# Optimization experiments

Hardware: AMD Instinct MI355X
Metric: run time of the kernel (lower is better)

Reference implementation:

```python
import jax, jax.numpy as jnp
import numpy as np

# ---- init_kwargs-derived constants ----
B, IN_F, OUT_F = 8192, 4096, 4096
W_SCALE = 0.01          # layer_params['w_scale']
B_SCALE = 0.01          # layer_params['b_scale']
IN_MIN, IN_MAX = -1.0, 1.0   # input_stats
NUM_BITS = 8
QMAX = 2 ** NUM_BITS - 1
IN_SCALE = (IN_MAX - IN_MIN) / QMAX
IN_ZP = int(round(-IN_MIN / (IN_SCALE + 1e-12)))


def setup_inputs() -> dict:
    key = jax.random.key(0)
    k1, k2, k3 = jax.random.split(key, 3)
    x_float = jax.random.normal(k1, (B, IN_F), dtype=jnp.float32)
    # int8-range weights/bias (stored as int32 containers)
    w_q = jax.random.randint(k2, (OUT_F, IN_F), -128, 128, dtype=jnp.int32)
    b_q = jax.random.randint(k3, (OUT_F,), -128, 128, dtype=jnp.int32)
    return {"x_float": x_float, "w_q": w_q, "b_q": b_q}


def reference(x_float, w_q, b_q):
    # quantize input to uint8 range [0,255]
    x_q = jnp.clip(jnp.round(x_float / IN_SCALE + IN_ZP), 0, 255).astype(jnp.int32)
    x_shifted = x_q - IN_ZP                       # [B, IN_F] int32
    # exact int32 accumulation matmul: [B, IN_F] @ [IN_F, OUT_F]
    acc_int = jnp.matmul(x_shifted, w_q.T, preferred_element_type=jnp.int32)
    out = acc_int.astype(jnp.float32) * (IN_SCALE * W_SCALE)
    out = out + b_q.astype(jnp.float32) * B_SCALE  # bias_float = b_q * b_scale
    return out
```

## Files before the change

### kernel.cpp

```cpp
#include <hip/hip_runtime.h>
#include <stdint.h>

constexpr int Mdim = 8192;
constexpr int Ndim = 4096;
constexpr int Kdim = 4096;

#define ISF        ((float)(2.0 / 255.0))
#define OUT_SCALE  ((float)(2.0 / 255.0 * 0.01))
#define BSCALE     0.01f

typedef int i32x4 __attribute__((ext_vector_type(4)));

__global__ __launch_bounds__(256) void quantize_x(const float* __restrict__ x,
                                                  int* __restrict__ x8,
                                                  int ngroups) {
  int idx = blockIdx.x * 256 + threadIdx.x;
  int stride = gridDim.x * 256;
  for (int g = idx; g < ngroups; g += stride) {
    float4 v = reinterpret_cast<const float4*>(x)[g];
    int a0 = (int)rintf(v.x / ISF + 127.0f);
    int a1 = (int)rintf(v.y / ISF + 127.0f);
    int a2 = (int)rintf(v.z / ISF + 127.0f);
    int a3 = (int)rintf(v.w / ISF + 127.0f);
    a0 = a0 < 0 ? 0 : (a0 > 255 ? 255 : a0); a0 -= 128;
    a1 = a1 < 0 ? 0 : (a1 > 255 ? 255 : a1); a1 -= 128;
    a2 = a2 < 0 ? 0 : (a2 > 255 ? 255 : a2); a2 -= 128;
    a3 = a3 < 0 ? 0 : (a3 > 255 ? 255 : a3); a3 -= 128;
    x8[g] = (a0 & 0xff) | ((a1 & 0xff) << 8) | ((a2 & 0xff) << 16) |
            (int)(((unsigned)(a3 & 0xff)) << 24);
  }
}

__global__ __launch_bounds__(256) void convert_w(const int* __restrict__ wq,
                                                 int* __restrict__ w8,
                                                 int* __restrict__ wsum) {
  int row = blockIdx.x;
  const int4* src = reinterpret_cast<const int4*>(wq + (size_t)row * Kdim);
  int* dst = w8 + (size_t)row * (Kdim / 4);
  int s = 0;
#pragma unroll
  for (int i = 0; i < 4; ++i) {
    int idx = i * 256 + threadIdx.x;
    int4 v = src[idx];
    s += v.x + v.y + v.z + v.w;
    dst[idx] = (v.x & 0xff) | ((v.y & 0xff) << 8) | ((v.z & 0xff) << 16) |
               (int)(((unsigned)(v.w & 0xff)) << 24);
  }
  __shared__ int red[256];
  red[threadIdx.x] = s;
  __syncthreads();
  for (int off = 128; off; off >>= 1) {
    if ((int)threadIdx.x < off) red[threadIdx.x] += red[threadIdx.x + off];
    __syncthreads();
  }
  if (threadIdx.x == 0) wsum[row] = red[0];
}

__global__ __launch_bounds__(256) void gemm_i8(const int8_t* __restrict__ A8,
                                               const int8_t* __restrict__ B8,
                                               const int* __restrict__ wsum,
                                               const int* __restrict__ bq,
                                               float* __restrict__ out) {
  __shared__ uint8_t lds[32768];

  int bid = blockIdx.x;
  int wg = (bid & 7) * 256 + (bid >> 3);
  int bm = wg >> 5;
  int bn = wg & 31;

  const int tid = threadIdx.x;
  const int lane = tid & 63;
  const int wv = tid >> 6;
  const int l15 = lane & 15, hi = lane >> 4;
  const int wr = wv >> 1, wc = wv & 1;
  const int sw = l15 & 7;

  size_t aSrc[4], bSrc[4];
  int ldsOff[4];
#pragma unroll
  for (int it = 0; it < 4; ++it) {
    int e = it * 256 + tid;
    int r = e >> 3, s = e & 7;
    int col = (s ^ (r & 7)) << 4;
    aSrc[it] = (size_t)(bm * 128 + r) * Kdim + col;
    bSrc[it] = (size_t)(bn * 128 + r) * Kdim + col;
    ldsOff[it] = it * 4096 + wv * 1024;
  }

  int aRow[4], bRow[4];
#pragma unroll
  for (int i = 0; i < 4; ++i) {
    aRow[i] = (wr * 64 + i * 16 + l15) * 128;
    bRow[i] = 16384 + (wc * 64 + i * 16 + l15) * 128;
  }

  i32x4 acc[4][4] = {};

  for (int kt = 0; kt < Kdim / 128; ++kt) {
#pragma unroll
    for (int it = 0; it < 4; ++it)
      __builtin_amdgcn_global_load_lds(
          (const __attribute__((address_space(1))) void*)(A8 + aSrc[it] + (size_t)kt * 128),
          (__attribute__((address_space(3))) void*)(&lds[ldsOff[it]]), 16, 0, 0);
#pragma unroll
    for (int it = 0; it < 4; ++it)
      __builtin_amdgcn_global_load_lds(
          (const __attribute__((address_space(1))) void*)(B8 + bSrc[it] + (size_t)kt * 128),
          (__attribute__((address_space(3))) void*)(&lds[16384 + ldsOff[it]]), 16, 0, 0);
    __syncthreads();

#pragma unroll
    for (int ks = 0; ks < 2; ++ks) {
      i32x4 a[4], b[4];
#pragma unroll
      for (int i = 0; i < 4; ++i)
        a[i] = *reinterpret_cast<const i32x4*>(&lds[aRow[i] + ((((ks << 2) + hi) ^ sw) << 4)]);
#pragma unroll
      for (int j = 0; j < 4; ++j)
        b[j] = *reinterpret_cast<const i32x4*>(&lds[bRow[j] + ((((ks << 2) + hi) ^ sw) << 4)]);
#pragma unroll
      for (int i = 0; i < 4; ++i)
#pragma unroll
        for (int j = 0; j < 4; ++j)
          acc[i][j] = __builtin_amdgcn_mfma_i32_16x16x64_i8(a[i], b[j], acc[i][j], 0, 0, 0);
    }
    __syncthreads();
  }

  float fb[4];
  int ws4[4];
#pragma unroll
  for (int j = 0; j < 4; ++j) {
    int c = bn * 128 + wc * 64 + j * 16 + l15;
    fb[j] = (float)bq[c] * BSCALE;
    ws4[j] = wsum[c];
  }
#pragma unroll
  for (int i = 0; i < 4; ++i) {
    int rbase = bm * 128 + wr * 64 + i * 16 + hi * 4;
#pragma unroll
    for (int p = 0; p < 4; ++p) {
      size_t ro = (size_t)(rbase + p) * Ndim + bn * 128 + wc * 64;
#pragma unroll
      for (int j = 0; j < 4; ++j)
        out[ro + j * 16 + l15] = (float)(acc[i][j][p] + ws4[j]) * OUT_SCALE + fb[j];
    }
  }
}

__global__ void fallback_kernel(const float* __restrict__ x, const int* __restrict__ wq,
                                const int* __restrict__ bq, float* __restrict__ out) {
  int col = blockIdx.x * 16 + (threadIdx.x & 15);
  int row = blockIdx.y * 16 + (threadIdx.x >> 4);
  const float* xr = x + (size_t)row * Kdim;
  const int* wr_ = wq + (size_t)col * Kdim;
  int acc = 0;
  for (int k = 0; k < Kdim; ++k) {
    int v = (int)rintf(xr[k] / ISF + 127.0f);
    v = v < 0 ? 0 : (v > 255 ? 255 : v);
    acc += (v - 127) * wr_[k];
  }
  out[(size_t)row * Ndim + col] = (float)acc * OUT_SCALE + (float)bq[col] * BSCALE;
}

extern "C" void kernel_launch(void* const* d_in, const int* in_sizes, int n_in,
                              void* d_out, int out_size, void* d_ws, size_t ws_size,
                              hipStream_t stream) {
  const float* x = (const float*)d_in[0];
  const int* wq = (const int*)d_in[1];
  const int* bq = (const int*)d_in[2];
  float* out = (float*)d_out;

  const size_t x8_bytes = (size_t)Mdim * Kdim;
  const size_t w8_bytes = (size_t)Ndim * Kdim;
  const size_t ws_need = x8_bytes + w8_bytes + (size_t)Ndim * sizeof(int);

  if (ws_size >= ws_need) {
    int8_t* x8 = (int8_t*)d_ws;
    int8_t* w8 = x8 + x8_bytes;
    int* wsum = (int*)(w8 + w8_bytes);

    quantize_x<<<2048, 256, 0, stream>>>(x, (int*)x8, Mdim * Kdim / 4);
    convert_w<<<Ndim, 256, 0, stream>>>(wq, (int*)w8, wsum);
    gemm_i8<<<(Mdim / 128) * (Ndim / 128), 256, 0, stream>>>(x8, w8, wsum, bq, out);
  } else {
    dim3 grid(Ndim / 16, Mdim / 16);
    fallback_kernel<<<grid, 256, 0, stream>>>(x, wq, bq, out);
  }
}
```

Measured before the change: 221.2 us.

## Rewrite int8 GEMM as 256x256 tile, double-buffered 8-phase pipelined kernel

Replaces the 128x128, 256-thread int8 GEMM with a 256x256 tile, 512-thread kernel. It uses 128KB of double-buffered LDS and splits each K tile into four phases. Prefetches for the next B tile and the A tile two steps ahead are issued between MFMA phases, paced with explicit vmcnt waits, barriers and s_setprio. The aim is to raise data reuse per loaded byte and hide global-to-LDS latency behind matrix work. The cost is much higher register and LDS pressure: one block per CU and only 512 workgroups, so about two waves across the device.

```diff
diff --git a/kernel.cpp b/kernel.cpp
--- a/kernel.cpp
+++ b/kernel.cpp
@@ -4,6 +4,7 @@
 constexpr int Mdim = 8192;
 constexpr int Ndim = 4096;
 constexpr int Kdim = 4096;
+constexpr int NT = Kdim / 128;
 
 #define ISF        ((float)(2.0 / 255.0))
 #define OUT_SCALE  ((float)(2.0 / 255.0 * 0.01))
@@ -56,96 +57,135 @@
   if (threadIdx.x == 0) wsum[row] = red[0];
 }
 
-__global__ __launch_bounds__(256) void gemm_i8(const int8_t* __restrict__ A8,
-                                               const int8_t* __restrict__ B8,
-                                               const int* __restrict__ wsum,
-                                               const int* __restrict__ bq,
-                                               float* __restrict__ out) {
-  __shared__ uint8_t lds[32768];
+#define AS1C const __attribute__((address_space(1))) void*
+#define AS3  __attribute__((address_space(3))) void*
+#define GLL(src, dst) __builtin_amdgcn_global_load_lds((AS1C)(src), (AS3)(dst), 16, 0, 0)
+#define BAR() asm volatile("s_barrier" ::: "memory")
+#define MFMA(a, b, c) __builtin_amdgcn_mfma_i32_16x16x64_i8(a, b, c, 0, 0, 0)
+
+__global__ __launch_bounds__(512) void gemm_i8_8ph(const int8_t* __restrict__ A8,
+                                                   const int8_t* __restrict__ B8,
+                                                   const int* __restrict__ wsum,
+                                                   const int* __restrict__ bq,
+                                                   float* __restrict__ out) {
+  __shared__ uint8_t lds[131072];
 
   int bid = blockIdx.x;
-  int wg = (bid & 7) * 256 + (bid >> 3);
-  int bm = wg >> 5;
-  int bn = wg & 31;
+  int wg = (bid & 7) * 64 + (bid >> 3);
+  int bm = wg >> 4;
+  int bn = wg & 15;
 
   const int tid = threadIdx.x;
   const int lane = tid & 63;
   const int wv = tid >> 6;
+  const int wr = wv >> 2;
+  const int wc = wv & 3;
   const int l15 = lane & 15, hi = lane >> 4;
-  const int wr = wv >> 1, wc = wv & 1;
-  const int sw = l15 & 7;
-
-  size_t aSrc[4], bSrc[4];
-  int ldsOff[4];
-#pragma unroll
-  for (int it = 0; it < 4; ++it) {
-    int e = it * 256 + tid;
-    int r = e >> 3, s = e & 7;
-    int col = (s ^ (r & 7)) << 4;
-    aSrc[it] = (size_t)(bm * 128 + r) * Kdim + col;
-    bSrc[it] = (size_t)(bn * 128 + r) * Kdim + col;
-    ldsOff[it] = it * 4096 + wv * 1024;
-  }
-
-  int aRow[4], bRow[4];
-#pragma unroll
-  for (int i = 0; i < 4; ++i) {
-    aRow[i] = (wr * 64 + i * 16 + l15) * 128;
-    bRow[i] = 16384 + (wc * 64 + i * 16 + l15) * 128;
-  }
-
-  i32x4 acc[4][4] = {};
-
-  for (int kt = 0; kt < Kdim / 128; ++kt) {
-#pragma unroll
-    for (int it = 0; it < 4; ++it)
-      __builtin_amdgcn_global_load_lds(
-          (const __attribute__((address_space(1))) void*)(A8 + aSrc[it] + (size_t)kt * 128),
-          (__attribute__((address_space(3))) void*)(&lds[ldsOff[it]]), 16, 0, 0);
-#pragma unroll
-    for (int it = 0; it < 4; ++it)
-      __builtin_amdgcn_global_load_lds(
-          (const __attribute__((address_space(1))) void*)(B8 + bSrc[it] + (size_t)kt * 128),
-          (__attribute__((address_space(3))) void*)(&lds[16384 + ldsOff[it]]), 16, 0, 0);
-    __syncthreads();
-
-#pragma unroll
-    for (int ks = 0; ks < 2; ++ks) {
-      i32x4 a[4], b[4];
-#pragma unroll
-      for (int i = 0; i < 4; ++i)
-        a[i] = *reinterpret_cast<const i32x4*>(&lds[aRow[i] + ((((ks << 2) + hi) ^ sw) << 4)]);
-#pragma unroll
-      for (int j = 0; j < 4; ++j)
-        b[j] = *reinterpret_cast<const i32x4*>(&lds[bRow[j] + ((((ks << 2) + hi) ^ sw) << 4)]);
-#pragma unroll
-      for (int i = 0; i < 4; ++i)
-#pragma unroll
-        for (int j = 0; j < 4; ++j)
-          acc[i][j] = __builtin_amdgcn_mfma_i32_16x16x64_i8(a[i], b[j], acc[i][j], 0, 0, 0);
+
+  const int r3 = lane >> 3, s3 = lane & 7;
+  const int swcol = (s3 ^ r3) << 4;
+  const size_t aoff = (size_t)(bm * 256 + wv * 8 + r3) * Kdim + swcol;
+  const size_t boff = (size_t)(bn * 256 + wv * 8 + r3) * Kdim + swcol;
+  const int ldsw = wv * 1024;
+
+#define ISSUE_A(P, t, half) do { \
+    GLL(A8 + aoff + (size_t)(t) * 128 + (size_t)((half) * 128) * Kdim, \
+        &lds[(P) * 32768 + (half) * 16384 + ldsw]); \
+    GLL(A8 + aoff + (size_t)(t) * 128 + (size_t)((half) * 128 + 64) * Kdim, \
+        &lds[(P) * 32768 + (half) * 16384 + 8192 + ldsw]); \
+  } while (0)
+#define ISSUE_B(P, t, half) do { \
+    GLL(B8 + boff + (size_t)(t) * 128 + (size_t)((half) * 128) * Kdim, \
+        &lds[65536 + (P) * 32768 + (half) * 16384 + ldsw]); \
+    GLL(B8 + boff + (size_t)(t) * 128 + (size_t)((half) * 128 + 64) * Kdim, \
+        &lds[65536 + (P) * 32768 + (half) * 16384 + 8192 + ldsw]); \
+  } while (0)
+
+  const int aRow = (wr * 128 + l15) * 128;
+  const int bRow = (wc * 64 + l15) * 128;
+  const int sl0 = (hi ^ (l15 & 7)) << 4;
+  const int sl1 = ((4 + hi) ^ (l15 & 7)) << 4;
+
+#define LDA(P, i, ks) (*reinterpret_cast<const i32x4*>( \
+    &lds[(P) * 32768 + aRow + (i) * 2048 + ((ks) ? sl1 : sl0)]))
+#define LDB(P, j, ks) (*reinterpret_cast<const i32x4*>( \
+    &lds[65536 + (P) * 32768 + bRow + (j) * 2048 + ((ks) ? sl1 : sl0)]))
+
+  i32x4 acc[8][4];
+#pragma unroll
+  for (int i = 0; i < 8; ++i)
+#pragma unroll
+    for (int j = 0; j < 4; ++j) acc[i][j] = (i32x4){0, 0, 0, 0};
+
+  ISSUE_A(0, 0, 0); ISSUE_A(0, 0, 1);
+  ISSUE_B(0, 0, 0); ISSUE_B(0, 0, 1);
+  ISSUE_A(1, 1, 0); ISSUE_A(1, 1, 1);
+  asm volatile("s_waitcnt vmcnt(4)" ::: "memory");
+  BAR();
+
+#define KTILE(P, t, DOB, DOA, VM4, VM0) do { \
+    i32x4 a0[8], a1[8], bb0, bb1; \
+     \
+    if (DOB) ISSUE_B((P) ^ 1, (t) + 1, 0); \
+    bb0 = LDB(P, 0, 0); bb1 = LDB(P, 1, 0); \
+    _Pragma("unroll") for (int i = 0; i < 8; ++i) a0[i] = LDA(P, i, 0); \
+    BAR(); __builtin_amdgcn_s_setprio(1); \
+    _Pragma("unroll") for (int i = 0; i < 8; ++i) { \
+      acc[i][0] = MFMA(a0[i], bb0, acc[i][0]); acc[i][1] = MFMA(a0[i], bb1, acc[i][1]); } \
+    __builtin_amdgcn_s_setprio(0); BAR(); \
+     \
+    if (DOB) ISSUE_B((P) ^ 1, (t) + 1, 1); \
+    bb0 = LDB(P, 2, 0); bb1 = LDB(P, 3, 0); \
+    _Pragma("unroll") for (int i = 0; i < 8; ++i) a1[i] = LDA(P, i, 1); \
+    BAR(); __builtin_amdgcn_s_setprio(1); \
+    _Pragma("unroll") for (int i = 0; i < 8; ++i) { \
+      acc[i][2] = MFMA(a0[i], bb0, acc[i][2]); acc[i][3] = MFMA(a0[i], bb1, acc[i][3]); } \
+    __builtin_amdgcn_s_setprio(0); BAR(); \
+     \
+    if (DOA) ISSUE_A(P, (t) + 2, 0); \
+    bb0 = LDB(P, 0, 1); bb1 = LDB(P, 1, 1); \
+    BAR(); __builtin_amdgcn_s_setprio(1); \
+    _Pragma("unroll") for (int i = 0; i < 8; ++i) { \
+      acc[i][0] = MFMA(a1[i], bb0, acc[i][0]); acc[i][1] = MFMA(a1[i], bb1, acc[i][1]); } \
+    __builtin_amdgcn_s_setprio(0); BAR(); \
+     \
+    if (DOA) ISSUE_A(P, (t) + 2, 1); \
+    bb0 = LDB(P, 2, 1); bb1 = LDB(P, 3, 1); \
+    BAR(); __builtin_amdgcn_s_setprio(1); \
+    _Pragma("unroll") for (int i = 0; i < 8; ++i) { \
+      acc[i][2] = MFMA(a1[i], bb0, acc[i][2]); acc[i][3] = MFMA(a1[i], bb1, acc[i][3]); } \
+    __builtin_amdgcn_s_setprio(0); \
+    if (VM4) asm volatile("s_waitcnt vmcnt(4)" ::: "memory"); \
+    if (VM0) asm volatile("s_waitcnt vmcnt(0)" ::: "memory"); \
+    BAR(); \
+  } while (0)
+
+  for (int it = 0; it < NT / 2 - 1; ++it) {
+    int ta = 2 * it, tb = 2 * it + 1;
+    KTILE(0, ta, 1, 1, 1, 0);
+    KTILE(1, tb, 1, 1, 1, 0);
+  }
+  KTILE(0, 30, 1, 0, 0, 1);
+  KTILE(1, 31, 0, 0, 0, 0);
+
+#pragma unroll
+  for (int j = 0; j < 4; ++j) {
+    int col = bn * 256 + wc * 64 + j * 16 + l15;
+    float fb = (float)bq[col] * BSCALE;
+    int ws = wsum[col];
+#pragma unroll
+    for (int i = 0; i < 8; ++i) {
+      int rbase = bm * 256 + wr * 128 + i * 16 + hi * 4;
+#pragma unroll
+      for (int p = 0; p < 4; ++p)
+        out[(size_t)(rbase + p) * Ndim + col] = (float)(acc[i][j][p] + ws) * OUT_SCALE + fb;
     }
-    __syncthreads();
-  }
-
-  float fb[4];
-  int ws4[4];
-#pragma unroll
-  for (int j = 0; j < 4; ++j) {
-    int c = bn * 128 + wc * 64 + j * 16 + l15;
-    fb[j] = (float)bq[c] * BSCALE;
-    ws4[j] = wsum[c];
-  }
-#pragma unroll
-  for (int i = 0; i < 4; ++i) {
-    int rbase = bm * 128 + wr * 64 + i * 16 + hi * 4;
-#pragma unroll
-    for (int p = 0; p < 4; ++p) {
-      size_t ro = (size_t)(rbase + p) * Ndim + bn * 128 + wc * 64;
-#pragma unroll
-      for (int j = 0; j < 4; ++j)
-        out[ro + j * 16 + l15] = (float)(acc[i][j][p] + ws4[j]) * OUT_SCALE + fb[j];
-    }
-  }
+  }
+#undef KTILE
+#undef ISSUE_A
+#undef ISSUE_B
+#undef LDA
+#undef LDB
 }
 
 __global__ void fallback_kernel(const float* __restrict__ x, const int* __restrict__ wq,
@@ -182,7 +222,7 @@
 
     quantize_x<<<2048, 256, 0, stream>>>(x, (int*)x8, Mdim * Kdim / 4);
     convert_w<<<Ndim, 256, 0, stream>>>(wq, (int*)w8, wsum);
-    gemm_i8<<<(Mdim / 128) * (Ndim / 128), 256, 0, stream>>>(x8, w8, wsum, bq, out);
+    gemm_i8_8ph<<<(Mdim / 256) * (Ndim / 256), 512, 0, stream>>>(x8, w8, wsum, bq, out);
   } else {
     dim3 grid(Ndim / 16, Mdim / 16);
     fallback_kernel<<<grid, 256, 0, stream>>>(x, wq, bq, out);
```

After: 179.2 us. 1.23x faster.
